# Kernel optimization log

Measured on AMD Instinct MI355X. Metric: run time of the kernel, lower is better.

Reference implementation:

```python
import math
import jax, jax.numpy as jnp
import numpy as np

D_MODEL = 1024
NUM_HEADS = 16
D_K = D_MODEL // NUM_HEADS
RANK = 16
B, L = 2, 2048


def setup_inputs() -> dict:
    key = jax.random.key(0)
    ks = jax.random.split(key, 10)
    w_scale = 0.02  # keep activations well-scaled like trained linears
    return {
        "x_q": jax.random.normal(ks[0], (B, L, D_MODEL), jnp.float32),
        "x_kv": jax.random.normal(ks[1], (B, L, D_MODEL), jnp.float32),
        "Wq": jax.random.normal(ks[2], (D_MODEL, D_MODEL), jnp.float32) * w_scale,
        "bq": jnp.zeros((D_MODEL,), jnp.float32),
        "Wk": jax.random.normal(ks[3], (D_MODEL, D_MODEL), jnp.float32) * w_scale,
        "bk": jnp.zeros((D_MODEL,), jnp.float32),
        "Wv": jax.random.normal(ks[4], (D_MODEL, D_MODEL), jnp.float32) * w_scale,
        "bv": jnp.zeros((D_MODEL,), jnp.float32),
        "Wo": jax.random.normal(ks[5], (D_MODEL, D_MODEL), jnp.float32) * w_scale,
        "bo": jnp.zeros((D_MODEL,), jnp.float32),
        "U_bil": jax.random.normal(ks[6], (NUM_HEADS, D_K, RANK), jnp.float32) * 0.02,
        "V_bil": jax.random.normal(ks[7], (NUM_HEADS, D_K, RANK), jnp.float32) * 0.02,
        "padding_mask": jnp.zeros((B, L), bool),  # True = padded KV position
    }


def reference(x_q, x_kv, Wq, bq, Wk, bk, Wv, bv, Wo, bo, U_bil, V_bil, padding_mask):
    b, l, _ = x_q.shape
    # torch nn.Linear: y = x @ W.T + b
    Q = (x_q @ Wq.T + bq).reshape(b, l, NUM_HEADS, D_K).transpose(0, 2, 1, 3)  # [B,H,L,dk]
    K = (x_kv @ Wk.T + bk).reshape(b, l, NUM_HEADS, D_K).transpose(0, 2, 1, 3)
    V = (x_kv @ Wv.T + bv).reshape(b, l, NUM_HEADS, D_K).transpose(0, 2, 1, 3)
    # low-rank bilinear projections: [B,H,L,rank]
    Q_proj = jnp.einsum("bhld,hdr->bhlr", Q, U_bil)
    K_proj = jnp.einsum("bhld,hdr->bhlr", K, V_bil)
    scores = jnp.einsum("bhqr,bhkr->bhqk", Q_proj, K_proj) / math.sqrt(RANK)  # [B,H,L,L]
    scores = jnp.where(padding_mask[:, None, None, :], jnp.float32(-10000.0), scores)
    attn = jax.nn.softmax(scores, axis=-1)  # dropout is identity in eval mode
    ctx = jnp.einsum("bhqk,bhkd->bhqd", attn, V)
    ctx = ctx.transpose(0, 2, 1, 3).reshape(b, l, D_MODEL)
    return ctx @ Wo.T + bo
```

## Files before the change

### kernel.cpp

```cpp
#include <hip/hip_runtime.h>
#include <hip/hip_bf16.h>

#define DM   1024
#define NH   16
#define DK   64
#define RK   16
#define BB   2
#define LL   2048
#define TT   (BB*LL)
#define HRK  256
#define NSPL 2


typedef float f4   __attribute__((ext_vector_type(4)));
typedef float f16v __attribute__((ext_vector_type(16)));
typedef short s8v  __attribute__((ext_vector_type(8)));
typedef unsigned int u2v __attribute__((ext_vector_type(2)));
typedef unsigned int u4v __attribute__((ext_vector_type(4)));

static __device__ __forceinline__ unsigned short f2b(float f) {
  __hip_bfloat16 h = __float2bfloat16(f);
  unsigned short u;
  __builtin_memcpy(&u, &h, 2);
  return u;
}
static __device__ __forceinline__ float b2f(unsigned short u) {
  __hip_bfloat16 h;
  __builtin_memcpy(&h, &u, 2);
  return __bfloat162float(h);
}

static __device__ __forceinline__ void gld_lds16(const void* g, void* l) {
  __builtin_amdgcn_global_load_lds(
      (const __attribute__((address_space(1))) unsigned int*)g,
      (__attribute__((address_space(3))) unsigned int*)l, 16, 0, 0);
}

__global__ __launch_bounds__(256) void cast_all(
    const float* __restrict__ s0, unsigned short* __restrict__ d0, int n0,
    const float* __restrict__ s1, unsigned short* __restrict__ d1, int n1,
    const float* __restrict__ s2, unsigned short* __restrict__ d2, int n2,
    const float* __restrict__ s3, unsigned short* __restrict__ d3, int n3) {
  const float* s; unsigned short* d; int n;
  switch (blockIdx.y) {
    case 0:  s = s0; d = d0; n = n0; break;
    case 1:  s = s1; d = d1; n = n1; break;
    case 2:  s = s2; d = d2; n = n2; break;
    default: s = s3; d = d3; n = n3; break;
  }
  for (int i = blockIdx.x*256 + threadIdx.x; i < n; i += gridDim.x*256) {
    const float4 v = ((const float4*)s)[i];
    ushort4 o;
    o.x = f2b(v.x); o.y = f2b(v.y); o.z = f2b(v.z); o.w = f2b(v.w);
    ((ushort4*)d)[i] = o;
  }
}

__global__ __launch_bounds__(256) void fuse_w(
    const float* __restrict__ Wq, const float* __restrict__ Wk,
    const float* __restrict__ Uq, const float* __restrict__ Uk,
    unsigned short* __restrict__ Aq, unsigned short* __restrict__ Ak) {
  const float* W = blockIdx.z ? Wk : Wq;
  const float* U = blockIdx.z ? Uk : Uq;
  unsigned short* At = blockIdx.z ? Ak : Aq;
  __shared__ float Us[64][16];
  __shared__ float Ws[4][64];
  const int i0 = blockIdx.x * 64;
  const int h  = blockIdx.y;
  const int tid = threadIdx.x;
  const int il = tid & 63, rr = tid >> 6;
  for (int t = tid; t < 64*16; t += 256)
    Us[t >> 4][t & 15] = U[(size_t)(h*DK + (t >> 4))*RK + (t & 15)];
  float acc[4] = {};
  for (int d0 = 0; d0 < DK; d0 += 4) {
    __syncthreads();
    Ws[rr][il] = W[(size_t)(h*DK + d0 + rr)*DM + i0 + il];
    __syncthreads();
#pragma unroll
    for (int dd = 0; dd < 4; ++dd) {
      const float w = Ws[dd][il];
#pragma unroll
      for (int j = 0; j < 4; ++j)
        acc[j] += w * Us[d0 + dd][rr*4 + j];
    }
  }
#pragma unroll
  for (int j = 0; j < 4; ++j)
    At[(size_t)(h*RK + rr*4 + j)*DM + i0 + il] = f2b(acc[j]);
}

__global__ void bias2(const float* __restrict__ bq, const float* __restrict__ bk,
                      const float* __restrict__ Uq, const float* __restrict__ Uk,
                      float* __restrict__ bpq, float* __restrict__ bpk) {
  const int t = threadIdx.x;
  const float* b = (t < 256) ? bq : bk;
  const float* U = (t < 256) ? Uq : Uk;
  float* bp = (t < 256) ? bpq : bpk;
  const int hr = t & 255, h = hr >> 4, r = hr & 15;
  float acc = 0.f;
  for (int d = 0; d < DK; ++d)
    acc += b[h*DK + d] * U[(size_t)(h*DK + d)*RK + r];
  bp[hr] = acc;
}

__global__ __launch_bounds__(256) void vsum_k(
    const unsigned short* __restrict__ Vt, float* __restrict__ Vsum4) {
  const int h = blockIdx.x, b = blockIdx.y, c = blockIdx.z;
  const int d = threadIdx.x >> 2, part = threadIdx.x & 3;
  const unsigned short* row =
      Vt + ((size_t)b*DM + h*DK + d)*LL + c*512 + part*128;
  float s = 0.f;
  for (int i = 0; i < 128; i += 8) {
    const s8v v = *(const s8v*)&row[i];
#pragma unroll
    for (int j = 0; j < 8; ++j) s += b2f((unsigned short)v[j]);
  }
  s += __shfl_xor(s, 1);
  s += __shfl_xor(s, 2);
  if (part == 0) Vsum4[(((size_t)c*BB + b)*NH + h)*DK + d] = s;
}

template<int N_, int MODE>
__global__ __launch_bounds__(256) void gemm64(
    const unsigned short* __restrict__ A0, const unsigned short* __restrict__ A1,
    const unsigned short* __restrict__ B0, const unsigned short* __restrict__ B1,
    const float* __restrict__ bi0, const float* __restrict__ bi1,
    void* __restrict__ C0, void* __restrict__ C1) {
  const unsigned short* Ag = blockIdx.z ? A1 : A0;
  const unsigned short* Bg = blockIdx.z ? B1 : B0;
  const float* bias = blockIdx.z ? bi1 : bi0;
  void* Cgv = blockIdx.z ? C1 : C0;
  __shared__ __align__(16) unsigned short Xs[64*32];
  __shared__ __align__(16) unsigned short Bs[128*32];
  const int t0 = blockIdx.x * 64, n0 = blockIdx.y * 128;
  const int tid = threadIdx.x, wave = tid >> 6, lane = tid & 63;
  const int quad = lane >> 4, l15 = lane & 15;
  const int nh = wave * 32;
  const int ar = tid >> 2, ac = (tid & 3) * 8;

  const f4 z = {0.f, 0.f, 0.f, 0.f};
  f4 acc[4][2];
#pragma unroll
  for (int a = 0; a < 4; ++a) { acc[a][0] = z; acc[a][1] = z; }

  for (int k0 = 0; k0 < DM; k0 += 32) {
    __syncthreads();
    gld_lds16(&Ag[(size_t)(t0 + ar)*DM + k0 + ac],       &Xs[wave*512]);
    gld_lds16(&Bg[(size_t)(n0 + ar)*DM + k0 + ac],       &Bs[wave*512]);
    gld_lds16(&Bg[(size_t)(n0 + 64 + ar)*DM + k0 + ac],  &Bs[2048 + wave*512]);
    __syncthreads();

    s8v af[4], bf[2];
#pragma unroll
    for (int ms = 0; ms < 4; ++ms)
      af[ms] = *(const s8v*)&Xs[(ms*16 + l15)*32 + quad*8];
#pragma unroll
    for (int ns = 0; ns < 2; ++ns)
      bf[ns] = *(const s8v*)&Bs[(nh + ns*16 + l15)*32 + quad*8];
#pragma unroll
    for (int ms = 0; ms < 4; ++ms)
#pragma unroll
      for (int ns = 0; ns < 2; ++ns)
        acc[ms][ns] = __builtin_amdgcn_mfma_f32_16x16x32_bf16(
            af[ms], bf[ns], acc[ms][ns], 0, 0, 0);
  }

#pragma unroll
  for (int ms = 0; ms < 4; ++ms) {
    const int tb = t0 + ms*16 + quad*4;
#pragma unroll
    for (int ns = 0; ns < 2; ++ns) {
      const int o = n0 + nh + ns*16 + l15;
      const float bv = bias[o];
      f4 a = acc[ms][ns];
      if (MODE == 1) {
        unsigned short* C = (unsigned short*)Cgv;
#pragma unroll
        for (int rg = 0; rg < 4; ++rg) {
          const int tt = tb + rg;
          C[(((size_t)(tt >> 11)*NH + (o >> 4))*LL + (tt & 2047))*RK + (o & 15)]
              = f2b(a[rg] + bv);
        }
      } else {
        float* C = (float*)Cgv;
#pragma unroll
        for (int rg = 0; rg < 4; ++rg)
          C[(size_t)(tb + rg)*N_ + o] = a[rg] + bv;
      }
    }
  }
}

template<int N_, int MODE>
__global__ __launch_bounds__(256) void gemm128(
    const unsigned short* __restrict__ Ag, const unsigned short* __restrict__ Bg,
    const float* __restrict__ bias, void* __restrict__ Cgv) {
  __shared__ __align__(16) unsigned short As[128*32];
  __shared__ __align__(16) unsigned short Bs[128*32];
  const int t0 = blockIdx.x * 128, n0 = blockIdx.y * 128;
  const int tid = threadIdx.x, wave = tid >> 6, lane = tid & 63;
  const int quad = lane >> 4, l15 = lane & 15;
  const int ar = tid >> 2, ac = (tid & 3) * 8;

  const f4 z = {0.f, 0.f, 0.f, 0.f};
  f4 acc[2][8];
#pragma unroll
  for (int m = 0; m < 2; ++m)
#pragma unroll
    for (int n = 0; n < 8; ++n) acc[m][n] = z;

  for (int k0 = 0; k0 < DM; k0 += 32) {
    __syncthreads();
    gld_lds16(&Ag[(size_t)(t0 + ar)*DM + k0 + ac],       &As[wave*512]);
    gld_lds16(&Ag[(size_t)(t0 + 64 + ar)*DM + k0 + ac],  &As[2048 + wave*512]);
    gld_lds16(&Bg[(size_t)(n0 + ar)*DM + k0 + ac],       &Bs[wave*512]);
    gld_lds16(&Bg[(size_t)(n0 + 64 + ar)*DM + k0 + ac],  &Bs[2048 + wave*512]);
    __syncthreads();

    s8v af[2], bf[8];
#pragma unroll
    for (int ms = 0; ms < 2; ++ms)
      af[ms] = *(const s8v*)&As[(wave*32 + ms*16 + l15)*32 + quad*8];
#pragma unroll
    for (int ns = 0; ns < 8; ++ns)
      bf[ns] = *(const s8v*)&Bs[(ns*16 + l15)*32 + quad*8];
#pragma unroll
    for (int ms = 0; ms < 2; ++ms)
#pragma unroll
      for (int ns = 0; ns < 8; ++ns)
        acc[ms][ns] = __builtin_amdgcn_mfma_f32_16x16x32_bf16(
            af[ms], bf[ns], acc[ms][ns], 0, 0, 0);
  }

#pragma unroll
  for (int ms = 0; ms < 2; ++ms) {
    const int tb = t0 + wave*32 + ms*16 + quad*4;
#pragma unroll
    for (int ns = 0; ns < 8; ++ns) {
      const int o = n0 + ns*16 + l15;
      const float bv = bias[o];
      f4 a = acc[ms][ns];
      if (MODE == 0) {
        float* C = (float*)Cgv;
#pragma unroll
        for (int rg = 0; rg < 4; ++rg)
          C[(size_t)(tb + rg)*N_ + o] = a[rg] + bv;
      } else {
        unsigned short* C = (unsigned short*)Cgv;
        const int bb = tb >> 11, l = tb & 2047;
        ushort4 pk;
        pk.x = f2b(a[0] + bv); pk.y = f2b(a[1] + bv);
        pk.z = f2b(a[2] + bv); pk.w = f2b(a[3] + bv);
        *(ushort4*)&C[((size_t)bb*DM + o)*LL + l] = pk;
      }
    }
  }
}

template<bool MASKED>
static __device__ __forceinline__ void softmax_pack(
    const f16v& s0, const f16v& s1, const unsigned long long mb, const int hi,
    float& den, unsigned int (&Pd)[2][4][2]) {
#pragma unroll
  for (int nt = 0; nt < 2; ++nt) {
    const f16v& sv = nt ? s1 : s0;
#pragma unroll
    for (int r = 0; r < 4; ++r) {
      float ep[4];
#pragma unroll
      for (int j = 0; j < 4; ++j) {
        float em = __expf(sv[r*4 + j] * 0.25f);
        if (MASKED) {
          const int kloc = nt*32 + j + 8*r + 4*hi;
          if ((mb >> kloc) & 1ull) em = 0.f;
        }
        den += em;
        ep[j] = em - 1.f;
      }
      asm("v_cvt_pk_bf16_f32 %0, %1, %2"
          : "=v"(Pd[nt][r][0]) : "v"(ep[0]), "v"(ep[1]));
      asm("v_cvt_pk_bf16_f32 %0, %1, %2"
          : "=v"(Pd[nt][r][1]) : "v"(ep[2]), "v"(ep[3]));
    }
  }
}

__global__ __launch_bounds__(256) void attention_v8(
    const unsigned short* __restrict__ Qp, const unsigned short* __restrict__ Kp,
    const unsigned short* __restrict__ Vt,
    const unsigned char* __restrict__ msk,
    unsigned short* __restrict__ P, float* __restrict__ denP) {
  __shared__ __align__(16) unsigned short Ks[2][2][64][8];
  __shared__ __align__(16) unsigned short Vs[2][8][64][8];
  const int q0 = blockIdx.x * 128, h = blockIdx.y;
  const int b = blockIdx.z & (BB - 1), ksp = blockIdx.z >> 1;
  const int kbeg = ksp * (LL / NSPL);
  const int NT = (LL / NSPL) / 64;
  const int tid = threadIdx.x, w = tid >> 6, lane = tid & 63;
  const int l31 = lane & 31, hi = lane >> 5;

  const s8v qfrag = *(const s8v*)&Qp[
      (((size_t)b*NH + h)*LL + q0 + w*32 + l31)*RK + hi*8];

  const int sr = tid >> 2, sp = tid & 3;
  const unsigned short* __restrict__ Vrow =
      Vt + ((size_t)b*DM + h*DK + sr)*LL + kbeg;
  const unsigned short* __restrict__ Kbase =
      Kp + (((size_t)b*NH + h)*LL + kbeg + sr)*RK + sp*4;
  const unsigned char*  __restrict__ Mrow = msk + (size_t)b*LL + kbeg + lane;

  u2v kpre; s8v vpre0, vpre1;
  unsigned char mcur, mnext;

  kpre  = *(const u2v*)&Kbase[0];
  vpre0 = *(const s8v*)&Vrow[sp*16];
  vpre1 = *(const s8v*)&Vrow[sp*16 + 8];
  mcur  = Mrow[0];
  *(u2v*)&Ks[0][sp>>1][sr][(sp&1)*4] = kpre;
  *(s8v*)&Vs[0][sp*2][sr][0]   = vpre0;
  *(s8v*)&Vs[0][sp*2+1][sr][0] = vpre1;
  kpre  = *(const u2v*)&Kbase[(size_t)64*RK];
  vpre0 = *(const s8v*)&Vrow[64 + sp*16];
  vpre1 = *(const s8v*)&Vrow[64 + sp*16 + 8];
  mnext = Mrow[64];
  __syncthreads();

  f16v acc0, acc1, z16;
#pragma unroll
  for (int i = 0; i < 16; ++i) { acc0[i] = 0.f; acc1[i] = 0.f; z16[i] = 0.f; }
  float den = 0.f;

  for (int t = 0; t < NT; ++t) {
    const int cur = t & 1;
    const unsigned long long mb = __ballot(mcur != 0);

    const s8v kf0 = *(const s8v*)&Ks[cur][hi][l31][0];
    const s8v kf1 = *(const s8v*)&Ks[cur][hi][32 + l31][0];

    const f16v s0 = __builtin_amdgcn_mfma_f32_32x32x16_bf16(kf0, qfrag, z16, 0, 0, 0);
    const f16v s1 = __builtin_amdgcn_mfma_f32_32x32x16_bf16(kf1, qfrag, z16, 0, 0, 0);

    unsigned int Pd[2][4][2];
    if (__builtin_expect(mb != 0ull, 0))
      softmax_pack<true >(s0, s1, mb, hi, den, Pd);
    else
      softmax_pack<false>(s0, s1, mb, hi, den, Pd);

#pragma unroll
    for (int kc = 0; kc < 4; ++kc) {
      const int nt = kc >> 1, a = (kc & 1)*2;
      const u2v r0 = __builtin_amdgcn_permlane32_swap(
          Pd[nt][a][0], Pd[nt][a+1][0], false, false);
      const u2v r1 = __builtin_amdgcn_permlane32_swap(
          Pd[nt][a][1], Pd[nt][a+1][1], false, false);
      u4v efi;
      efi[0] = r0[0];
      efi[1] = r1[0];
      efi[2] = r0[1];
      efi[3] = r1[1];
      const s8v ef = __builtin_bit_cast(s8v, efi);
      const s8v vf0 = *(const s8v*)&Vs[cur][kc*2 + hi][l31][0];
      const s8v vf1 = *(const s8v*)&Vs[cur][kc*2 + hi][32 + l31][0];
      acc0 = __builtin_amdgcn_mfma_f32_32x32x16_bf16(ef, vf0, acc0, 0, 0, 0);
      acc1 = __builtin_amdgcn_mfma_f32_32x32x16_bf16(ef, vf1, acc1, 0, 0, 0);
    }

    if (t + 1 < NT) {
      *(u2v*)&Ks[cur^1][sp>>1][sr][(sp&1)*4] = kpre;
      *(s8v*)&Vs[cur^1][sp*2][sr][0]   = vpre0;
      *(s8v*)&Vs[cur^1][sp*2+1][sr][0] = vpre1;
      const int tn = (t + 2 < NT) ? t + 2 : NT - 1;
      kpre  = *(const u2v*)&Kbase[(size_t)tn*64*RK];
      vpre0 = *(const s8v*)&Vrow[tn*64 + sp*16];
      vpre1 = *(const s8v*)&Vrow[tn*64 + sp*16 + 8];
      mcur  = mnext;
      mnext = Mrow[tn*64];
    }
    __syncthreads();
  }

  den += __shfl_xor(den, 32);
  if (hi == 0)
    denP[(((size_t)ksp*BB + b)*NH + h)*LL + q0 + w*32 + l31] = den;

#pragma unroll
  for (int rg = 0; rg < 16; ++rg) {
    const int qr = (rg & 3) + 8*(rg >> 2) + 4*hi;
    const size_t base = 2*(((size_t)(b*LL + q0 + w*32 + qr))*DM + h*DK) + ksp;
    P[base + 2*l31]        = f2b(acc0[rg]);
    P[base + 2*(32 + l31)] = f2b(acc1[rg]);
  }
}

__global__ __launch_bounds__(256) void reduce_k(
    const unsigned int* __restrict__ P, const float* __restrict__ Vsum4,
    const float* __restrict__ denP, unsigned short* __restrict__ ctxb) {
  const size_t j0 = ((size_t)blockIdx.x*256 + threadIdx.x)*4;
  const int t  = (int)(j0 >> 10);
  const int dm = (int)(j0 & 1023);
  const int b = t >> 11, l = t & 2047;
  const int h = dm >> 6, d = dm & 63;
  const float dn =
      denP[((size_t)b*NH + h)*LL + l] +
      denP[(((size_t)BB + b)*NH + h)*LL + l];
  const float inv = 1.f / fmaxf(dn, 1e-30f);
  f4 vs = {0.f, 0.f, 0.f, 0.f};
#pragma unroll
  for (int c = 0; c < 4; ++c) {
    const f4 v = *(const f4*)&Vsum4[(((size_t)c*BB + b)*NH + h)*DK + d];
    vs[0] += v[0]; vs[1] += v[1]; vs[2] += v[2]; vs[3] += v[3];
  }
  const u4v p = *(const u4v*)&P[j0];
  ushort4 pk;
  float c0 = (vs[0] + b2f((unsigned short)(p[0] & 0xffff))
                    + b2f((unsigned short)(p[0] >> 16))) * inv;
  float c1 = (vs[1] + b2f((unsigned short)(p[1] & 0xffff))
                    + b2f((unsigned short)(p[1] >> 16))) * inv;
  float c2 = (vs[2] + b2f((unsigned short)(p[2] & 0xffff))
                    + b2f((unsigned short)(p[2] >> 16))) * inv;
  float c3 = (vs[3] + b2f((unsigned short)(p[3] & 0xffff))
                    + b2f((unsigned short)(p[3] >> 16))) * inv;
  pk.x = f2b(c0); pk.y = f2b(c1); pk.z = f2b(c2); pk.w = f2b(c3);
  *(ushort4*)&ctxb[j0] = pk;
}

extern "C" void kernel_launch(void* const* d_in, const int* in_sizes, int n_in,
                              void* d_out, int out_size, void* d_ws, size_t ws_size,
                              hipStream_t stream) {
  (void)in_sizes; (void)n_in; (void)out_size; (void)ws_size;
  const float* x_q   = (const float*)d_in[0];
  const float* x_kv  = (const float*)d_in[1];
  const float* Wq    = (const float*)d_in[2];
  const float* bq    = (const float*)d_in[3];
  const float* Wk    = (const float*)d_in[4];
  const float* bk    = (const float*)d_in[5];
  const float* Wv    = (const float*)d_in[6];
  const float* bv    = (const float*)d_in[7];
  const float* Wo    = (const float*)d_in[8];
  const float* bo    = (const float*)d_in[9];
  const float* U_bil = (const float*)d_in[10];
  const float* V_bil = (const float*)d_in[11];
  const unsigned char* pmask = (const unsigned char*)d_in[12];
  float* out = (float*)d_out;

  char* w = (char*)d_ws;
  unsigned short* xq_b  = (unsigned short*)(w);
  unsigned short* xkv_b = (unsigned short*)(w +  8388608);
  unsigned short* Wv_b  = (unsigned short*)(w + 16777216);
  unsigned short* Wo_b  = (unsigned short*)(w + 18874368);
  unsigned short* Atq   = (unsigned short*)(w + 20971520);
  unsigned short* Atk   = (unsigned short*)(w + 21495808);
  float*          bpq   = (float*)(w + 22020096);
  float*          bpk   = (float*)(w + 22021120);
  unsigned short* Qp    = (unsigned short*)(w + 22022144);
  unsigned short* Kp    = (unsigned short*)(w + 24119296);
  unsigned short* Vt    = (unsigned short*)(w + 26216448);
  float*          denP  = (float*)(w + 34613248);
  float*          Vsum4 = (float*)(w + 35137536);
  unsigned short* Pbuf  = (unsigned short*)w;
  unsigned short* ctxb  = Vt;

  cast_all<<<dim3(1024, 4), 256, 0, stream>>>(
      x_q, xq_b, TT*DM/4, x_kv, xkv_b, TT*DM/4,
      Wv, Wv_b, DM*DM/4,  Wo, Wo_b, DM*DM/4);
  fuse_w<<<dim3(DM/64, NH, 2), 256, 0, stream>>>(Wq, Wk, U_bil, V_bil, Atq, Atk);
  bias2<<<1, 512, 0, stream>>>(bq, bk, U_bil, V_bil, bpq, bpk);
  gemm64<HRK, 1><<<dim3(64, 2, 2), 256, 0, stream>>>(
      xq_b, xkv_b, Atq, Atk, bpq, bpk, Qp, Kp);
  gemm128<DM, 2><<<dim3(32, 8), 256, 0, stream>>>(xkv_b, Wv_b, bv, Vt);
  vsum_k<<<dim3(NH, BB, 4), 256, 0, stream>>>(Vt, Vsum4);
  attention_v8<<<dim3(LL/128, NH, BB*NSPL), 256, 0, stream>>>(
      Qp, Kp, Vt, pmask, Pbuf, denP);
  reduce_k<<<dim3(TT*DM/1024), 256, 0, stream>>>(
      (const unsigned int*)w, Vsum4, denP, ctxb);
  gemm128<DM, 0><<<dim3(32, 8), 256, 0, stream>>>(ctxb, Wo_b, bo, out);
}
```

Before: 255.5 us.

## Merge prep, projection, attention and output stages into four fused kernels

Merges the cast, weight-fusion and bias kernels into one prep launch. The Q/K low-rank projections and the V projection now share one launch, V row-sums are computed by extra blocks inside the attention launch, and the split-K reduce is folded into the A-operand load of the output GEMM. This cuts the launch count from nine to four and removes the separate reduce pass along with its ctx write/read round trip. In exchange, the output GEMM uses a 64-row tile and does per-element conversion work in its load loop. Work also overlaps differently across launches.

```diff
diff --git a/kernel.cpp b/kernel.cpp
--- a/kernel.cpp
+++ b/kernel.cpp
@@ -8,7 +8,6 @@
 #define BB   2
 #define LL   2048
 #define TT   (BB*LL)
-#define HRK  256
 #define NSPL 2
 
 
@@ -36,19 +35,10 @@
       (__attribute__((address_space(3))) unsigned int*)l, 16, 0, 0);
 }
 
-__global__ __launch_bounds__(256) void cast_all(
-    const float* __restrict__ s0, unsigned short* __restrict__ d0, int n0,
-    const float* __restrict__ s1, unsigned short* __restrict__ d1, int n1,
-    const float* __restrict__ s2, unsigned short* __restrict__ d2, int n2,
-    const float* __restrict__ s3, unsigned short* __restrict__ d3, int n3) {
-  const float* s; unsigned short* d; int n;
-  switch (blockIdx.y) {
-    case 0:  s = s0; d = d0; n = n0; break;
-    case 1:  s = s1; d = d1; n = n1; break;
-    case 2:  s = s2; d = d2; n = n2; break;
-    default: s = s3; d = d3; n = n3; break;
-  }
-  for (int i = blockIdx.x*256 + threadIdx.x; i < n; i += gridDim.x*256) {
+static __device__ __forceinline__ void cast_rng(
+    const float* __restrict__ s, unsigned short* __restrict__ d,
+    int n4, int lb, int nb, int tid) {
+  for (int i = lb*256 + tid; i < n4; i += nb*256) {
     const float4 v = ((const float4*)s)[i];
     ushort4 o;
     o.x = f2b(v.x); o.y = f2b(v.y); o.z = f2b(v.z); o.w = f2b(v.w);
@@ -56,202 +46,171 @@
   }
 }
 
-__global__ __launch_bounds__(256) void fuse_w(
-    const float* __restrict__ Wq, const float* __restrict__ Wk,
-    const float* __restrict__ Uq, const float* __restrict__ Uk,
-    unsigned short* __restrict__ Aq, unsigned short* __restrict__ Ak) {
-  const float* W = blockIdx.z ? Wk : Wq;
-  const float* U = blockIdx.z ? Uk : Uq;
-  unsigned short* At = blockIdx.z ? Ak : Aq;
-  __shared__ float Us[64][16];
-  __shared__ float Ws[4][64];
-  const int i0 = blockIdx.x * 64;
-  const int h  = blockIdx.y;
-  const int tid = threadIdx.x;
-  const int il = tid & 63, rr = tid >> 6;
-  for (int t = tid; t < 64*16; t += 256)
-    Us[t >> 4][t & 15] = U[(size_t)(h*DK + (t >> 4))*RK + (t & 15)];
-  float acc[4] = {};
-  for (int d0 = 0; d0 < DK; d0 += 4) {
-    __syncthreads();
-    Ws[rr][il] = W[(size_t)(h*DK + d0 + rr)*DM + i0 + il];
-    __syncthreads();
-#pragma unroll
-    for (int dd = 0; dd < 4; ++dd) {
-      const float w = Ws[dd][il];
-#pragma unroll
-      for (int j = 0; j < 4; ++j)
-        acc[j] += w * Us[d0 + dd][rr*4 + j];
-    }
-  }
-#pragma unroll
-  for (int j = 0; j < 4; ++j)
-    At[(size_t)(h*RK + rr*4 + j)*DM + i0 + il] = f2b(acc[j]);
-}
-
-__global__ void bias2(const float* __restrict__ bq, const float* __restrict__ bk,
-                      const float* __restrict__ Uq, const float* __restrict__ Uk,
-                      float* __restrict__ bpq, float* __restrict__ bpk) {
-  const int t = threadIdx.x;
-  const float* b = (t < 256) ? bq : bk;
-  const float* U = (t < 256) ? Uq : Uk;
-  float* bp = (t < 256) ? bpq : bpk;
-  const int hr = t & 255, h = hr >> 4, r = hr & 15;
-  float acc = 0.f;
-  for (int d = 0; d < DK; ++d)
-    acc += b[h*DK + d] * U[(size_t)(h*DK + d)*RK + r];
-  bp[hr] = acc;
-}
-
-__global__ __launch_bounds__(256) void vsum_k(
-    const unsigned short* __restrict__ Vt, float* __restrict__ Vsum4) {
-  const int h = blockIdx.x, b = blockIdx.y, c = blockIdx.z;
-  const int d = threadIdx.x >> 2, part = threadIdx.x & 3;
-  const unsigned short* row =
-      Vt + ((size_t)b*DM + h*DK + d)*LL + c*512 + part*128;
-  float s = 0.f;
-  for (int i = 0; i < 128; i += 8) {
-    const s8v v = *(const s8v*)&row[i];
-#pragma unroll
-    for (int j = 0; j < 8; ++j) s += b2f((unsigned short)v[j]);
-  }
-  s += __shfl_xor(s, 1);
-  s += __shfl_xor(s, 2);
-  if (part == 0) Vsum4[(((size_t)c*BB + b)*NH + h)*DK + d] = s;
-}
-
-template<int N_, int MODE>
-__global__ __launch_bounds__(256) void gemm64(
-    const unsigned short* __restrict__ A0, const unsigned short* __restrict__ A1,
-    const unsigned short* __restrict__ B0, const unsigned short* __restrict__ B1,
-    const float* __restrict__ bi0, const float* __restrict__ bi1,
-    void* __restrict__ C0, void* __restrict__ C1) {
-  const unsigned short* Ag = blockIdx.z ? A1 : A0;
-  const unsigned short* Bg = blockIdx.z ? B1 : B0;
-  const float* bias = blockIdx.z ? bi1 : bi0;
-  void* Cgv = blockIdx.z ? C1 : C0;
-  __shared__ __align__(16) unsigned short Xs[64*32];
-  __shared__ __align__(16) unsigned short Bs[128*32];
-  const int t0 = blockIdx.x * 64, n0 = blockIdx.y * 128;
-  const int tid = threadIdx.x, wave = tid >> 6, lane = tid & 63;
+__global__ __launch_bounds__(256) void prep_k(
+    const float* __restrict__ xq,  const float* __restrict__ xkv,
+    const float* __restrict__ Wv,  const float* __restrict__ Wo,
+    unsigned short* __restrict__ xq_b,  unsigned short* __restrict__ xkv_b,
+    unsigned short* __restrict__ Wv_b,  unsigned short* __restrict__ Wo_b,
+    const float* __restrict__ Wq,  const float* __restrict__ Wk,
+    const float* __restrict__ Uq,  const float* __restrict__ Uk,
+    unsigned short* __restrict__ Aq, unsigned short* __restrict__ Ak,
+    const float* __restrict__ bq,  const float* __restrict__ bk,
+    float* __restrict__ bpq, float* __restrict__ bpk) {
+  __shared__ float sh[64*16 + 4*64];
+  const int x = blockIdx.x, tid = threadIdx.x;
+  if (x < 1024) {
+    cast_rng(xq,  xq_b,  TT*DM/4, x,        1024, tid);
+  } else if (x < 2048) {
+    cast_rng(xkv, xkv_b, TT*DM/4, x - 1024, 1024, tid);
+  } else if (x < 2304) {
+    cast_rng(Wv,  Wv_b,  DM*DM/4, x - 2048, 256, tid);
+  } else if (x < 2560) {
+    cast_rng(Wo,  Wo_b,  DM*DM/4, x - 2304, 256, tid);
+  } else if (x < 3072) {
+    const int fidx = x - 2560;
+    const int sel = fidx >> 8, f = fidx & 255;
+    const float* W = sel ? Wk : Wq;
+    const float* U = sel ? Uk : Uq;
+    unsigned short* At = sel ? Ak : Aq;
+    const int i0 = (f & 15) * 64, h = f >> 4;
+    float* Us = sh;
+    float* Ws = sh + 1024;
+    const int il = tid & 63, rr = tid >> 6;
+    for (int t = tid; t < 64*16; t += 256)
+      Us[t] = U[(size_t)(h*DK + (t >> 4))*RK + (t & 15)];
+    float acc[4] = {};
+    for (int d0 = 0; d0 < DK; d0 += 4) {
+      __syncthreads();
+      Ws[rr*64 + il] = W[(size_t)(h*DK + d0 + rr)*DM + i0 + il];
+      __syncthreads();
+#pragma unroll
+      for (int dd = 0; dd < 4; ++dd) {
+        const float w = Ws[dd*64 + il];
+#pragma unroll
+        for (int j = 0; j < 4; ++j)
+          acc[j] += w * Us[(d0 + dd)*16 + rr*4 + j];
+      }
+    }
+#pragma unroll
+    for (int j = 0; j < 4; ++j)
+      At[(size_t)(h*RK + rr*4 + j)*DM + i0 + il] = f2b(acc[j]);
+  } else {
+    const int h = tid >> 4, r = tid & 15;
+    float aq = 0.f, ak = 0.f;
+    for (int d = 0; d < DK; ++d) {
+      aq += bq[h*DK + d] * Uq[(size_t)(h*DK + d)*RK + r];
+      ak += bk[h*DK + d] * Uk[(size_t)(h*DK + d)*RK + r];
+    }
+    bpq[tid] = aq; bpk[tid] = ak;
+  }
+}
+
+__global__ __launch_bounds__(256) void proj_k(
+    const unsigned short* __restrict__ xq_b, const unsigned short* __restrict__ xkv_b,
+    const unsigned short* __restrict__ Atq,  const unsigned short* __restrict__ Atk,
+    const float* __restrict__ bpq, const float* __restrict__ bpk,
+    unsigned short* __restrict__ Qp, unsigned short* __restrict__ Kp,
+    const unsigned short* __restrict__ Wv_b, const float* __restrict__ bv,
+    unsigned short* __restrict__ Vt) {
+  __shared__ __align__(16) unsigned short shm[8192];
+  const int f = blockIdx.x, tid = threadIdx.x;
+  const int wave = tid >> 6, lane = tid & 63;
   const int quad = lane >> 4, l15 = lane & 15;
-  const int nh = wave * 32;
   const int ar = tid >> 2, ac = (tid & 3) * 8;
-
   const f4 z = {0.f, 0.f, 0.f, 0.f};
-  f4 acc[4][2];
-#pragma unroll
-  for (int a = 0; a < 4; ++a) { acc[a][0] = z; acc[a][1] = z; }
-
-  for (int k0 = 0; k0 < DM; k0 += 32) {
-    __syncthreads();
-    gld_lds16(&Ag[(size_t)(t0 + ar)*DM + k0 + ac],       &Xs[wave*512]);
-    gld_lds16(&Bg[(size_t)(n0 + ar)*DM + k0 + ac],       &Bs[wave*512]);
-    gld_lds16(&Bg[(size_t)(n0 + 64 + ar)*DM + k0 + ac],  &Bs[2048 + wave*512]);
-    __syncthreads();
-
-    s8v af[4], bf[2];
-#pragma unroll
-    for (int ms = 0; ms < 4; ++ms)
-      af[ms] = *(const s8v*)&Xs[(ms*16 + l15)*32 + quad*8];
-#pragma unroll
-    for (int ns = 0; ns < 2; ++ns)
-      bf[ns] = *(const s8v*)&Bs[(nh + ns*16 + l15)*32 + quad*8];
-#pragma unroll
-    for (int ms = 0; ms < 4; ++ms)
+
+  if (f < 256) {
+    const int xb = f & 63, yb = (f >> 6) & 1, zb = f >> 7;
+    const unsigned short* Ag = zb ? xkv_b : xq_b;
+    const unsigned short* Bg = zb ? Atk : Atq;
+    const float* bias = zb ? bpk : bpq;
+    unsigned short* C = zb ? Kp : Qp;
+    unsigned short* Xs = shm;
+    unsigned short* Bs = shm + 2048;
+    const int t0 = xb*64, n0 = yb*128, nh = wave*32;
+    f4 acc[4][2];
+#pragma unroll
+    for (int a = 0; a < 4; ++a) { acc[a][0] = z; acc[a][1] = z; }
+    for (int k0 = 0; k0 < DM; k0 += 32) {
+      __syncthreads();
+      gld_lds16(&Ag[(size_t)(t0 + ar)*DM + k0 + ac],      &Xs[wave*512]);
+      gld_lds16(&Bg[(size_t)(n0 + ar)*DM + k0 + ac],      &Bs[wave*512]);
+      gld_lds16(&Bg[(size_t)(n0 + 64 + ar)*DM + k0 + ac], &Bs[2048 + wave*512]);
+      __syncthreads();
+      s8v af[4], bf[2];
+#pragma unroll
+      for (int ms = 0; ms < 4; ++ms)
+        af[ms] = *(const s8v*)&Xs[(ms*16 + l15)*32 + quad*8];
 #pragma unroll
       for (int ns = 0; ns < 2; ++ns)
-        acc[ms][ns] = __builtin_amdgcn_mfma_f32_16x16x32_bf16(
-            af[ms], bf[ns], acc[ms][ns], 0, 0, 0);
-  }
-
-#pragma unroll
-  for (int ms = 0; ms < 4; ++ms) {
-    const int tb = t0 + ms*16 + quad*4;
-#pragma unroll
-    for (int ns = 0; ns < 2; ++ns) {
-      const int o = n0 + nh + ns*16 + l15;
-      const float bv = bias[o];
-      f4 a = acc[ms][ns];
-      if (MODE == 1) {
-        unsigned short* C = (unsigned short*)Cgv;
+        bf[ns] = *(const s8v*)&Bs[(nh + ns*16 + l15)*32 + quad*8];
+#pragma unroll
+      for (int ms = 0; ms < 4; ++ms)
+#pragma unroll
+        for (int ns = 0; ns < 2; ++ns)
+          acc[ms][ns] = __builtin_amdgcn_mfma_f32_16x16x32_bf16(
+              af[ms], bf[ns], acc[ms][ns], 0, 0, 0);
+    }
+#pragma unroll
+    for (int ms = 0; ms < 4; ++ms) {
+      const int tb = t0 + ms*16 + quad*4;
+#pragma unroll
+      for (int ns = 0; ns < 2; ++ns) {
+        const int o = n0 + nh + ns*16 + l15;
+        const float bvv = bias[o];
+        f4 a = acc[ms][ns];
 #pragma unroll
         for (int rg = 0; rg < 4; ++rg) {
           const int tt = tb + rg;
           C[(((size_t)(tt >> 11)*NH + (o >> 4))*LL + (tt & 2047))*RK + (o & 15)]
-              = f2b(a[rg] + bv);
+              = f2b(a[rg] + bvv);
         }
-      } else {
-        float* C = (float*)Cgv;
-#pragma unroll
-        for (int rg = 0; rg < 4; ++rg)
-          C[(size_t)(tb + rg)*N_ + o] = a[rg] + bv;
       }
     }
-  }
-}
-
-template<int N_, int MODE>
-__global__ __launch_bounds__(256) void gemm128(
-    const unsigned short* __restrict__ Ag, const unsigned short* __restrict__ Bg,
-    const float* __restrict__ bias, void* __restrict__ Cgv) {
-  __shared__ __align__(16) unsigned short As[128*32];
-  __shared__ __align__(16) unsigned short Bs[128*32];
-  const int t0 = blockIdx.x * 128, n0 = blockIdx.y * 128;
-  const int tid = threadIdx.x, wave = tid >> 6, lane = tid & 63;
-  const int quad = lane >> 4, l15 = lane & 15;
-  const int ar = tid >> 2, ac = (tid & 3) * 8;
-
-  const f4 z = {0.f, 0.f, 0.f, 0.f};
-  f4 acc[2][8];
-#pragma unroll
-  for (int m = 0; m < 2; ++m)
-#pragma unroll
-    for (int n = 0; n < 8; ++n) acc[m][n] = z;
-
-  for (int k0 = 0; k0 < DM; k0 += 32) {
-    __syncthreads();
-    gld_lds16(&Ag[(size_t)(t0 + ar)*DM + k0 + ac],       &As[wave*512]);
-    gld_lds16(&Ag[(size_t)(t0 + 64 + ar)*DM + k0 + ac],  &As[2048 + wave*512]);
-    gld_lds16(&Bg[(size_t)(n0 + ar)*DM + k0 + ac],       &Bs[wave*512]);
-    gld_lds16(&Bg[(size_t)(n0 + 64 + ar)*DM + k0 + ac],  &Bs[2048 + wave*512]);
-    __syncthreads();
-
-    s8v af[2], bf[8];
-#pragma unroll
-    for (int ms = 0; ms < 2; ++ms)
-      af[ms] = *(const s8v*)&As[(wave*32 + ms*16 + l15)*32 + quad*8];
-#pragma unroll
-    for (int ns = 0; ns < 8; ++ns)
-      bf[ns] = *(const s8v*)&Bs[(ns*16 + l15)*32 + quad*8];
-#pragma unroll
-    for (int ms = 0; ms < 2; ++ms)
+  } else {
+    const int g = f - 256, gx = g & 31, gy = g >> 5;
+    unsigned short* As = shm;
+    unsigned short* Bs = shm + 4096;
+    const int t0 = gx*128, n0 = gy*128;
+    f4 acc[2][8];
+#pragma unroll
+    for (int m = 0; m < 2; ++m)
+#pragma unroll
+      for (int n = 0; n < 8; ++n) acc[m][n] = z;
+    for (int k0 = 0; k0 < DM; k0 += 32) {
+      __syncthreads();
+      gld_lds16(&xkv_b[(size_t)(t0 + ar)*DM + k0 + ac],      &As[wave*512]);
+      gld_lds16(&xkv_b[(size_t)(t0 + 64 + ar)*DM + k0 + ac], &As[2048 + wave*512]);
+      gld_lds16(&Wv_b[(size_t)(n0 + ar)*DM + k0 + ac],       &Bs[wave*512]);
+      gld_lds16(&Wv_b[(size_t)(n0 + 64 + ar)*DM + k0 + ac],  &Bs[2048 + wave*512]);
+      __syncthreads();
+      s8v af[2], bf[8];
+#pragma unroll
+      for (int ms = 0; ms < 2; ++ms)
+        af[ms] = *(const s8v*)&As[(wave*32 + ms*16 + l15)*32 + quad*8];
 #pragma unroll
       for (int ns = 0; ns < 8; ++ns)
-        acc[ms][ns] = __builtin_amdgcn_mfma_f32_16x16x32_bf16(
-            af[ms], bf[ns], acc[ms][ns], 0, 0, 0);
-  }
-
-#pragma unroll
-  for (int ms = 0; ms < 2; ++ms) {
-    const int tb = t0 + wave*32 + ms*16 + quad*4;
-#pragma unroll
-    for (int ns = 0; ns < 8; ++ns) {
-      const int o = n0 + ns*16 + l15;
-      const float bv = bias[o];
-      f4 a = acc[ms][ns];
-      if (MODE == 0) {
-        float* C = (float*)Cgv;
-#pragma unroll
-        for (int rg = 0; rg < 4; ++rg)
-          C[(size_t)(tb + rg)*N_ + o] = a[rg] + bv;
-      } else {
-        unsigned short* C = (unsigned short*)Cgv;
+        bf[ns] = *(const s8v*)&Bs[(ns*16 + l15)*32 + quad*8];
+#pragma unroll
+      for (int ms = 0; ms < 2; ++ms)
+#pragma unroll
+        for (int ns = 0; ns < 8; ++ns)
+          acc[ms][ns] = __builtin_amdgcn_mfma_f32_16x16x32_bf16(
+              af[ms], bf[ns], acc[ms][ns], 0, 0, 0);
+    }
+#pragma unroll
+    for (int ms = 0; ms < 2; ++ms) {
+      const int tb = t0 + wave*32 + ms*16 + quad*4;
+#pragma unroll
+      for (int ns = 0; ns < 8; ++ns) {
+        const int o = n0 + ns*16 + l15;
+        const float bvv = bv[o];
+        f4 a = acc[ms][ns];
         const int bb = tb >> 11, l = tb & 2047;
         ushort4 pk;
-        pk.x = f2b(a[0] + bv); pk.y = f2b(a[1] + bv);
-        pk.z = f2b(a[2] + bv); pk.w = f2b(a[3] + bv);
-        *(ushort4*)&C[((size_t)bb*DM + o)*LL + l] = pk;
+        pk.x = f2b(a[0] + bvv); pk.y = f2b(a[1] + bvv);
+        pk.z = f2b(a[2] + bvv); pk.w = f2b(a[3] + bvv);
+        *(ushort4*)&Vt[((size_t)bb*DM + o)*LL + l] = pk;
       }
     }
   }
@@ -285,18 +244,38 @@
   }
 }
 
-__global__ __launch_bounds__(256) void attention_v8(
+__global__ __launch_bounds__(256) void attn_k(
     const unsigned short* __restrict__ Qp, const unsigned short* __restrict__ Kp,
     const unsigned short* __restrict__ Vt,
     const unsigned char* __restrict__ msk,
-    unsigned short* __restrict__ P, float* __restrict__ denP) {
+    unsigned short* __restrict__ P, float* __restrict__ denP,
+    float* __restrict__ Vsum) {
   __shared__ __align__(16) unsigned short Ks[2][2][64][8];
   __shared__ __align__(16) unsigned short Vs[2][8][64][8];
+  const int tid = threadIdx.x;
+
+  if (blockIdx.z == 4) {
+    if (blockIdx.y >= BB) return;
+    const int h = blockIdx.x, b = blockIdx.y;
+    const int d = tid >> 2, part = tid & 3;
+    const unsigned short* row = Vt + ((size_t)b*DM + h*DK + d)*LL + part*512;
+    float s = 0.f;
+    for (int i = 0; i < 512; i += 8) {
+      const s8v v = *(const s8v*)&row[i];
+#pragma unroll
+      for (int j = 0; j < 8; ++j) s += b2f((unsigned short)v[j]);
+    }
+    s += __shfl_xor(s, 1);
+    s += __shfl_xor(s, 2);
+    if (part == 0) Vsum[((size_t)b*NH + h)*DK + d] = s;
+    return;
+  }
+
   const int q0 = blockIdx.x * 128, h = blockIdx.y;
   const int b = blockIdx.z & (BB - 1), ksp = blockIdx.z >> 1;
   const int kbeg = ksp * (LL / NSPL);
   const int NT = (LL / NSPL) / 64;
-  const int tid = threadIdx.x, w = tid >> 6, lane = tid & 63;
+  const int w = tid >> 6, lane = tid & 63;
   const int l31 = lane & 31, hi = lane >> 5;
 
   const s8v qfrag = *(const s8v*)&Qp[
@@ -386,42 +365,90 @@
 #pragma unroll
   for (int rg = 0; rg < 16; ++rg) {
     const int qr = (rg & 3) + 8*(rg >> 2) + 4*hi;
-    const size_t base = 2*(((size_t)(b*LL + q0 + w*32 + qr))*DM + h*DK) + ksp;
-    P[base + 2*l31]        = f2b(acc0[rg]);
-    P[base + 2*(32 + l31)] = f2b(acc1[rg]);
-  }
-}
-
-__global__ __launch_bounds__(256) void reduce_k(
-    const unsigned int* __restrict__ P, const float* __restrict__ Vsum4,
-    const float* __restrict__ denP, unsigned short* __restrict__ ctxb) {
-  const size_t j0 = ((size_t)blockIdx.x*256 + threadIdx.x)*4;
-  const int t  = (int)(j0 >> 10);
-  const int dm = (int)(j0 & 1023);
-  const int b = t >> 11, l = t & 2047;
-  const int h = dm >> 6, d = dm & 63;
-  const float dn =
-      denP[((size_t)b*NH + h)*LL + l] +
-      denP[(((size_t)BB + b)*NH + h)*LL + l];
-  const float inv = 1.f / fmaxf(dn, 1e-30f);
-  f4 vs = {0.f, 0.f, 0.f, 0.f};
-#pragma unroll
-  for (int c = 0; c < 4; ++c) {
-    const f4 v = *(const f4*)&Vsum4[(((size_t)c*BB + b)*NH + h)*DK + d];
-    vs[0] += v[0]; vs[1] += v[1]; vs[2] += v[2]; vs[3] += v[3];
-  }
-  const u4v p = *(const u4v*)&P[j0];
-  ushort4 pk;
-  float c0 = (vs[0] + b2f((unsigned short)(p[0] & 0xffff))
-                    + b2f((unsigned short)(p[0] >> 16))) * inv;
-  float c1 = (vs[1] + b2f((unsigned short)(p[1] & 0xffff))
-                    + b2f((unsigned short)(p[1] >> 16))) * inv;
-  float c2 = (vs[2] + b2f((unsigned short)(p[2] & 0xffff))
-                    + b2f((unsigned short)(p[2] >> 16))) * inv;
-  float c3 = (vs[3] + b2f((unsigned short)(p[3] & 0xffff))
-                    + b2f((unsigned short)(p[3] >> 16))) * inv;
-  pk.x = f2b(c0); pk.y = f2b(c1); pk.z = f2b(c2); pk.w = f2b(c3);
-  *(ushort4*)&ctxb[j0] = pk;
+    const size_t pbase =
+        ((size_t)ksp*TT + b*LL + q0 + w*32 + qr)*DM + h*DK;
+    P[pbase + l31]      = f2b(acc0[rg]);
+    P[pbase + 32 + l31] = f2b(acc1[rg]);
+  }
+}
+
+__global__ __launch_bounds__(256) void outred_k(
+    const unsigned short* __restrict__ P, const float* __restrict__ Vsum,
+    const float* __restrict__ denP, const unsigned short* __restrict__ Bg,
+    const float* __restrict__ bias, float* __restrict__ C) {
+  __shared__ __align__(16) unsigned short Xs[64*32];
+  __shared__ __align__(16) unsigned short Bs[128*32];
+  const int f = blockIdx.x;
+  const int t0 = (f & 63) * 64, n0 = (f >> 6) * 128;
+  const int tid = threadIdx.x, wave = tid >> 6, lane = tid & 63;
+  const int quad = lane >> 4, l15 = lane & 15;
+  const int nh = wave * 32;
+  const int ar = tid >> 2, ac = (tid & 3) * 8;
+  const int trow = t0 + ar;
+  const int b = trow >> 11, l = trow & 2047;
+  const unsigned short* __restrict__ P0 = P + (size_t)trow*DM;
+  const unsigned short* __restrict__ P1 = P + ((size_t)TT + trow)*DM;
+  const float* __restrict__ vsb = Vsum + (size_t)b*DM;
+  const float* __restrict__ dp0 = denP + ((size_t)b*NH)*LL + l;
+  const float* __restrict__ dp1 = denP + (((size_t)BB + b)*NH)*LL + l;
+
+  const f4 z = {0.f, 0.f, 0.f, 0.f};
+  f4 acc[4][2];
+#pragma unroll
+  for (int a = 0; a < 4; ++a) { acc[a][0] = z; acc[a][1] = z; }
+
+  for (int k0 = 0; k0 < DM; k0 += 32) {
+    __syncthreads();
+    gld_lds16(&Bg[(size_t)(n0 + ar)*DM + k0 + ac],      &Bs[wave*512]);
+    gld_lds16(&Bg[(size_t)(n0 + 64 + ar)*DM + k0 + ac], &Bs[2048 + wave*512]);
+    const int hk = k0 >> 6;
+    const float dn = dp0[(size_t)hk*LL] + dp1[(size_t)hk*LL];
+    const float inv = 1.f / fmaxf(dn, 1e-30f);
+    const s8v p0 = *(const s8v*)&P0[k0 + ac];
+    const s8v p1 = *(const s8v*)&P1[k0 + ac];
+    const f4 vs0 = *(const f4*)&vsb[k0 + ac];
+    const f4 vs1 = *(const f4*)&vsb[k0 + ac + 4];
+    s8v av;
+#pragma unroll
+    for (int j = 0; j < 4; ++j) {
+      const float c0 = (vs0[j] + b2f((unsigned short)p0[j])
+                               + b2f((unsigned short)p1[j])) * inv;
+      const float c1 = (vs1[j] + b2f((unsigned short)p0[4+j])
+                               + b2f((unsigned short)p1[4+j])) * inv;
+      av[j]     = (short)f2b(c0);
+      av[4 + j] = (short)f2b(c1);
+    }
+    *(s8v*)&Xs[ar*32 + ac] = av;
+    __syncthreads();
+
+    s8v af[4], bf[2];
+#pragma unroll
+    for (int ms = 0; ms < 4; ++ms)
+      af[ms] = *(const s8v*)&Xs[(ms*16 + l15)*32 + quad*8];
+#pragma unroll
+    for (int ns = 0; ns < 2; ++ns)
+      bf[ns] = *(const s8v*)&Bs[(nh + ns*16 + l15)*32 + quad*8];
+#pragma unroll
+    for (int ms = 0; ms < 4; ++ms)
+#pragma unroll
+      for (int ns = 0; ns < 2; ++ns)
+        acc[ms][ns] = __builtin_amdgcn_mfma_f32_16x16x32_bf16(
+            af[ms], bf[ns], acc[ms][ns], 0, 0, 0);
+  }
+
+#pragma unroll
+  for (int ms = 0; ms < 4; ++ms) {
+    const int tb = t0 + ms*16 + quad*4;
+#pragma unroll
+    for (int ns = 0; ns < 2; ++ns) {
+      const int o = n0 + nh + ns*16 + l15;
+      const float bv = bias[o];
+      f4 a = acc[ms][ns];
+#pragma unroll
+      for (int rg = 0; rg < 4; ++rg)
+        C[(size_t)(tb + rg)*DM + o] = a[rg] + bv;
+    }
+  }
 }
 
 extern "C" void kernel_launch(void* const* d_in, const int* in_sizes, int n_in,
@@ -455,23 +482,16 @@
   unsigned short* Qp    = (unsigned short*)(w + 22022144);
   unsigned short* Kp    = (unsigned short*)(w + 24119296);
   unsigned short* Vt    = (unsigned short*)(w + 26216448);
+  float*          Vsum  = (float*)(w + 34605056);
   float*          denP  = (float*)(w + 34613248);
-  float*          Vsum4 = (float*)(w + 35137536);
   unsigned short* Pbuf  = (unsigned short*)w;
-  unsigned short* ctxb  = Vt;
-
-  cast_all<<<dim3(1024, 4), 256, 0, stream>>>(
-      x_q, xq_b, TT*DM/4, x_kv, xkv_b, TT*DM/4,
-      Wv, Wv_b, DM*DM/4,  Wo, Wo_b, DM*DM/4);
-  fuse_w<<<dim3(DM/64, NH, 2), 256, 0, stream>>>(Wq, Wk, U_bil, V_bil, Atq, Atk);
-  bias2<<<1, 512, 0, stream>>>(bq, bk, U_bil, V_bil, bpq, bpk);
-  gemm64<HRK, 1><<<dim3(64, 2, 2), 256, 0, stream>>>(
-      xq_b, xkv_b, Atq, Atk, bpq, bpk, Qp, Kp);
-  gemm128<DM, 2><<<dim3(32, 8), 256, 0, stream>>>(xkv_b, Wv_b, bv, Vt);
-  vsum_k<<<dim3(NH, BB, 4), 256, 0, stream>>>(Vt, Vsum4);
-  attention_v8<<<dim3(LL/128, NH, BB*NSPL), 256, 0, stream>>>(
-      Qp, Kp, Vt, pmask, Pbuf, denP);
-  reduce_k<<<dim3(TT*DM/1024), 256, 0, stream>>>(
-      (const unsigned int*)w, Vsum4, denP, ctxb);
-  gemm128<DM, 0><<<dim3(32, 8), 256, 0, stream>>>(ctxb, Wo_b, bo, out);
-}
+
+  prep_k<<<3073, 256, 0, stream>>>(
+      x_q, x_kv, Wv, Wo, xq_b, xkv_b, Wv_b, Wo_b,
+      Wq, Wk, U_bil, V_bil, Atq, Atk, bq, bk, bpq, bpk);
+  proj_k<<<512, 256, 0, stream>>>(
+      xq_b, xkv_b, Atq, Atk, bpq, bpk, Qp, Kp, Wv_b, bv, Vt);
+  attn_k<<<dim3(LL/128, NH, 5), 256, 0, stream>>>(
+      Qp, Kp, Vt, pmask, Pbuf, denP, Vsum);
+  outred_k<<<512, 256, 0, stream>>>(Pbuf, Vsum, denP, Wo_b, bo, out);
+}
```

Measured after the change: 226.1 us. 11.5% less time.
